# Performance work log

Hardware: AMD Instinct MI355X
Metric: run time of the kernel (lower is better)

The kernel has to match this reference:

```python
import jax, jax.numpy as jnp
import numpy as np

B, S, D, H = 4, 2048, 1024, 16
DH = D // H
NEG = -10000.0


def setup_inputs() -> dict:
    key = jax.random.key(0)
    ks = jax.random.split(key, 12)
    scale = 0.02
    inp = {
        "q": jax.random.normal(ks[0], (B, S, D), jnp.float32),
        "k": jax.random.normal(ks[1], (B, S, D), jnp.float32),
        "v": jax.random.normal(ks[2], (B, S, D), jnp.float32),
        "mask": jnp.triu(jnp.ones((S, S), jnp.bool_), k=1),  # True = masked (causal)
        "Wq": jax.random.normal(ks[3], (D, D), jnp.float32) * scale,
        "bq": jnp.zeros((D,), jnp.float32),
        "Wk": jax.random.normal(ks[4], (D, D), jnp.float32) * scale,
        "bk": jnp.zeros((D,), jnp.float32),
        "Wv": jax.random.normal(ks[5], (D, D), jnp.float32) * scale,
        "bv": jnp.zeros((D,), jnp.float32),
        "Wo": jax.random.normal(ks[6], (D, D), jnp.float32) * scale,
        "bo": jnp.zeros((D,), jnp.float32),
    }
    return inp


def _split(x):
    # [B,S,D] -> [B,H,S,DH]
    return x.reshape(B, S, H, DH).transpose(0, 2, 1, 3)


def reference(q, k, v, mask, Wq, bq, Wk, bk, Wv, bv, Wo, bo):
    # torch Linear: y = x @ W.T + b
    qh = _split(q @ Wq.T + bq)
    kh = _split(k @ Wk.T + bk)
    vh = _split(v @ Wv.T + bv)
    # scaled dot-product scores: [B,H,S,S]
    scores = jnp.einsum("bhqd,bhkd->bhqk", qh, kh) / jnp.sqrt(jnp.float32(DH))
    scores = scores + jnp.where(mask, jnp.float32(NEG), jnp.float32(0.0))
    attn = jax.nn.softmax(scores, axis=-1)  # dropout_rate=0 -> identity
    out = jnp.einsum("bhqk,bhkd->bhqd", attn, vh)
    out = out.transpose(0, 2, 1, 3).reshape(B, S, D)
    return out @ Wo.T + bo
```

## Files before the change

kernel.cpp:

```cpp
#include <hip/hip_runtime.h>
#include <hip/hip_bf16.h>


#define B_ 4
#define S_ 2048
#define D_ 1024
#define H_ 16
#define DH_ 64
#define M_ (B_*S_)
#define MASKADD (-14427.0f)
#define QSCALE  (0.180336880f)

typedef __attribute__((ext_vector_type(8)))  __bf16 bf16x8;
typedef __attribute__((ext_vector_type(8)))  unsigned short ushort8;
typedef __attribute__((ext_vector_type(4)))  float f32x4;
typedef __attribute__((ext_vector_type(16))) float f32x16;

__device__ __forceinline__ unsigned short f2bf(float f) {
  __hip_bfloat16 h = __float2bfloat16(f);
  union { __hip_bfloat16 h; unsigned short u; } c; c.h = h; return c.u;
}

__device__ __forceinline__ f32x4 mfma16(bf16x8 a, bf16x8 b, f32x4 c) {
  return __builtin_amdgcn_mfma_f32_16x16x32_bf16(a, b, c, 0, 0, 0);
}
__device__ __forceinline__ f32x16 mfma32(bf16x8 a, bf16x8 b, f32x16 c) {
  return __builtin_amdgcn_mfma_f32_32x32x16_bf16(a, b, c, 0, 0, 0);
}

__device__ __forceinline__ unsigned cvtpk(float lo, float hi) {
  unsigned r;
  asm("v_cvt_pk_bf16_f32 %0, %1, %2" : "=v"(r) : "v"(lo), "v"(hi));
  return r;
}

__device__ __forceinline__ void gld_lds16(const void* g, void* l) {
  __builtin_amdgcn_global_load_lds(
      (const __attribute__((address_space(1))) unsigned int*)g,
      (__attribute__((address_space(3))) unsigned int*)l, 16, 0, 0);
}

__global__ void cvt4_kernel(const float* __restrict__ p0, const float* __restrict__ p1,
                            const float* __restrict__ p2, const float* __restrict__ p3,
                            unsigned short* __restrict__ o0, unsigned short* __restrict__ o1,
                            unsigned short* __restrict__ o2, unsigned short* __restrict__ o3,
                            int n4) {
  int i = blockIdx.x * blockDim.x + threadIdx.x;
  if (i >= n4) return;
  const float* in  = (blockIdx.y == 0) ? p0 : (blockIdx.y == 1 ? p1 : (blockIdx.y == 2 ? p2 : p3));
  unsigned short* out = (blockIdx.y == 0) ? o0 : (blockIdx.y == 1 ? o1 : (blockIdx.y == 2 ? o2 : o3));
  float4 f = reinterpret_cast<const float4*>(in)[i];
  ushort4 o;
  o.x = f2bf(f.x); o.y = f2bf(f.y); o.z = f2bf(f.z); o.w = f2bf(f.w);
  reinterpret_cast<ushort4*>(out)[i] = o;
}

template<bool F32A>
__device__ __forceinline__
void gemm_body(const void* __restrict__ Ap, const unsigned short* __restrict__ W,
               const float* __restrict__ bias, void* __restrict__ outp,
               int mode, bool sc,
               unsigned short (*sA)[128*32], unsigned short (*sB)[128*32])
{
  const int tid  = threadIdx.x;
  const int lane = tid & 63, wid = tid >> 6;
  const int bx = blockIdx.x;
  const int j8 = bx & 7, i8 = bx >> 3;
  const int mt = j8*8 + (i8 >> 3), nt = i8 & 7;
  const int m0 = mt*128, n0 = nt*128;
  const int wr = wid >> 1, wc = wid & 1;

  const float* A32 = (const float*)Ap;
  const unsigned short* A16 = (const unsigned short*)Ap;

  f32x4 acc[4][4];
  #pragma unroll
  for (int i = 0; i < 4; ++i)
    #pragma unroll
    for (int j = 0; j < 4; ++j)
      #pragma unroll
      for (int r = 0; r < 4; ++r) acc[i][j][r] = 0.0f;

  auto stageB = [&](int bufi, int kt) {
    const unsigned short* Wb = W + (size_t)n0*D_ + kt*32;
    #pragma unroll
    for (int p = 0; p < 2; ++p) {
      int r = 32*wid + 16*p + (lane >> 2);
      int c = (lane & 3) * 8;
      gld_lds16(Wb + (size_t)r*D_ + c, &sB[bufi][(32*wid + 16*p)*32]);
    }
  };
  auto stageA16 = [&](int bufi, int kt) {
    const unsigned short* Ab = A16 + (size_t)m0*D_ + kt*32;
    #pragma unroll
    for (int p = 0; p < 2; ++p) {
      int r = 32*wid + 16*p + (lane >> 2);
      int c = (lane & 3) * 8;
      gld_lds16(Ab + (size_t)r*D_ + c, &sA[bufi][(32*wid + 16*p)*32]);
    }
  };

  f32x4 fr[4];
  auto loadA32 = [&](int kt) {
    const float* p = A32 + (size_t)(m0 + (tid >> 1))*D_ + kt*32 + (tid & 1)*16;
    fr[0] = *(const f32x4*)(p);
    fr[1] = *(const f32x4*)(p + 4);
    fr[2] = *(const f32x4*)(p + 8);
    fr[3] = *(const f32x4*)(p + 12);
  };
  auto writeA32 = [&](int bufi) {
    ushort8 o0, o1;
    #pragma unroll
    for (int j = 0; j < 4; ++j) {
      o0[j]   = f2bf(fr[0][j]);
      o0[4+j] = f2bf(fr[1][j]);
      o1[j]   = f2bf(fr[2][j]);
      o1[4+j] = f2bf(fr[3][j]);
    }
    unsigned short* dst = &sA[bufi][(tid >> 1)*32 + (tid & 1)*16];
    *(ushort8*)dst       = o0;
    *(ushort8*)(dst + 8) = o1;
  };

  if (F32A) { loadA32(0); writeA32(0); }
  else      { stageA16(0, 0); }
  stageB(0, 0);

  const int NK = D_/32;
  int buf = 0;
  for (int kt = 0; kt < NK; ++kt) {
    __syncthreads();
    bf16x8 aF[4], bF[4];
    #pragma unroll
    for (int i = 0; i < 4; ++i)
      aF[i] = *(const bf16x8*)&sA[buf][(64*wr + 16*i + (lane & 15))*32 + (lane >> 4)*8];
    #pragma unroll
    for (int j = 0; j < 4; ++j)
      bF[j] = *(const bf16x8*)&sB[buf][(64*wc + 16*j + (lane & 15))*32 + (lane >> 4)*8];

    if (kt + 1 < NK) {
      if (F32A) loadA32(kt + 1);
      else      stageA16(buf ^ 1, kt + 1);
      stageB(buf ^ 1, kt + 1);
    }

    #pragma unroll
    for (int i = 0; i < 4; ++i)
      #pragma unroll
      for (int j = 0; j < 4; ++j)
        acc[i][j] = mfma16(aF[i], bF[j], acc[i][j]);

    if (F32A && kt + 1 < NK) writeA32(buf ^ 1);
    buf ^= 1;
  }

  #pragma unroll
  for (int i = 0; i < 4; ++i) {
    int gr0 = m0 + 64*wr + 16*i + ((lane >> 4) << 2);
    #pragma unroll
    for (int j = 0; j < 4; ++j) {
      int gc = n0 + 64*wc + 16*j + (lane & 15);
      float bv = bias[gc];
      if (mode == 2) {
        int b = gr0 >> 11, s = gr0 & (S_ - 1);
        int hh = gc >> 6, dh = gc & (DH_ - 1);
        ushort4 o;
        o.x = f2bf(acc[i][j][0] + bv); o.y = f2bf(acc[i][j][1] + bv);
        o.z = f2bf(acc[i][j][2] + bv); o.w = f2bf(acc[i][j][3] + bv);
        *(ushort4*)&((unsigned short*)outp)[(((size_t)b*H_ + hh)*DH_ + dh)*S_ + s] = o;
      } else {
        #pragma unroll
        for (int r = 0; r < 4; ++r) {
          float v = acc[i][j][r] + bv;
          if (sc) v *= QSCALE;
          int gr = gr0 + r;
          if (mode == 0) {
            int b = gr >> 11, s = gr & (S_ - 1);
            int hh = gc >> 6, dh = gc & (DH_ - 1);
            ((unsigned short*)outp)[(((size_t)b*H_ + hh)*S_ + s)*DH_ + dh] = f2bf(v);
          } else {
            ((float*)outp)[(size_t)gr*D_ + gc] = v;
          }
        }
      }
    }
  }
}

__global__ __launch_bounds__(256, 2)
void gemm_qkv(const float* __restrict__ Aq, const float* __restrict__ Ak,
              const float* __restrict__ Av,
              const unsigned short* __restrict__ Wq_, const unsigned short* __restrict__ Wk_,
              const unsigned short* __restrict__ Wv_,
              const float* __restrict__ bq_, const float* __restrict__ bk_,
              const float* __restrict__ bv_,
              unsigned short* __restrict__ Oq, unsigned short* __restrict__ Ok,
              unsigned short* __restrict__ Ov)
{
  __shared__ unsigned short sA[2][128*32];
  __shared__ unsigned short sB[2][128*32];
  const int y = blockIdx.y;
  const float* A = (y == 0) ? Aq : (y == 1 ? Ak : Av);
  const unsigned short* W = (y == 0) ? Wq_ : (y == 1 ? Wk_ : Wv_);
  const float* bias        = (y == 0) ? bq_ : (y == 1 ? bk_ : bv_);
  unsigned short* outp     = (y == 0) ? Oq  : (y == 1 ? Ok  : Ov);
  gemm_body<true>(A, W, bias, outp, (y == 2) ? 2 : 0, y == 0, sA, sB);
}

__global__ __launch_bounds__(256, 2)
void gemm_out(const unsigned short* __restrict__ A, const unsigned short* __restrict__ W,
              const float* __restrict__ bias, float* __restrict__ outp)
{
  __shared__ unsigned short sA[2][128*32];
  __shared__ unsigned short sB[2][128*32];
  gemm_body<false>(A, W, bias, outp, 1, false, sA, sB);
}

__global__ __launch_bounds__(256)
void attn_kernel(const unsigned short* __restrict__ Qh, const unsigned short* __restrict__ Kh,
                 const unsigned short* __restrict__ Vt, unsigned short* __restrict__ AO)
{
  __shared__ unsigned short sK [2][64*64];
  __shared__ unsigned short sVt[2][64*64];

  const int tid = threadIdx.x, lane = tid & 63, wid = tid >> 6;
  const int l31 = lane & 31, h5 = lane >> 5;
  const int bh = blockIdx.x;
  const int chunk = 15 - (int)blockIdx.y;
  const int bb = bh >> 4, hd = bh & 15;
  const unsigned short* Qb = Qh + (size_t)bh * S_ * DH_;
  const unsigned short* Kb = Kh + (size_t)bh * S_ * DH_;
  const unsigned short* Vb = Vt + (size_t)bh * DH_ * S_;
  const int qc0 = chunk * 128;
  const int NT  = 2*chunk + 2;
  const int qw0 = qc0 + wid*32;
  const int q   = qw0 + l31;

  bf16x8 qF[4];
  #pragma unroll
  for (int c = 0; c < 4; ++c)
    qF[c] = *(const bf16x8*)(Qb + (size_t)q*DH_ + c*16 + h5*8);

  f32x16 zz;
  #pragma unroll
  for (int r = 0; r < 16; ++r) zz[r] = 0.0f;
  f32x16 accO0 = zz, accO1 = zz;
  float lsum = 0.0f;

  auto stageK = [&](int bufi, int t) {
    #pragma unroll
    for (int p = 0; p < 2; ++p) {
      int ch = 2*wid + p;
      int row = ch*8 + (lane >> 3);
      int cbs = ((lane & 7) * 16) ^ ((row & 7) << 4);
      gld_lds16(Kb + (size_t)(t*64 + row)*DH_ + (cbs >> 1), &sK[bufi][ch*512]);
    }
  };
  auto stageV = [&](int bufi, int t) {
    #pragma unroll
    for (int p = 0; p < 2; ++p) {
      int ch = 2*wid + p;
      int row = ch*8 + (lane >> 3);
      int cbs = ((lane & 7) * 16) ^ ((row & 7) << 4);
      gld_lds16(Vb + (size_t)row*S_ + t*64 + (cbs >> 1), &sVt[bufi][ch*512]);
    }
  };

  stageK(0, 0);
  stageV(0, 0);

  int buf = 0;
  for (int t = 0; t < NT; ++t) {
    __syncthreads();
    if (t + 1 < NT) { stageK(buf ^ 1, t + 1); stageV(buf ^ 1, t + 1); }

    #pragma unroll
    for (int sub = 0; sub < 2; ++sub) {
      const int kv0 = t*64 + sub*32;
      if (kv0 > qw0 + 31) continue;
      const bool dodiag = (kv0 + 31 > qw0);

      f32x16 st = zz;
      __builtin_amdgcn_s_setprio(1);
      #pragma unroll
      for (int c = 0; c < 4; ++c) {
        int row = sub*32 + l31;
        const char* base = (const char*)&sK[buf][0] + row*128;
        bf16x8 kf = *(const bf16x8*)(base + ((32*c + 16*h5) ^ ((row & 7) << 4)));
        st = mfma32(kf, qF[c], st);
      }
      __builtin_amdgcn_s_setprio(0);

      #pragma unroll
      for (int r = 0; r < 16; ++r) {
        float x = st[r];
        if (dodiag) {
          int kv = kv0 + (r & 3) + 8*(r >> 2) + 4*h5;
          if (kv > q) x += MASKADD;
        }
        x = __builtin_amdgcn_exp2f(x);
        st[r] = x;
        lsum += x;
      }

      #pragma unroll
      for (int hh = 0; hh < 2; ++hh) {
        union { unsigned u[4]; bf16x8 v; } pb;
        pb.u[0] = cvtpk(st[8*hh+0], st[8*hh+1]);
        pb.u[1] = cvtpk(st[8*hh+2], st[8*hh+3]);
        pb.u[2] = cvtpk(st[8*hh+4], st[8*hh+5]);
        pb.u[3] = cvtpk(st[8*hh+6], st[8*hh+7]);

        __builtin_amdgcn_s_setprio(1);
        #pragma unroll
        for (int dh = 0; dh < 2; ++dh) {
          int row = dh*32 + l31;
          const char* base = (const char*)&sVt[buf][0] + row*128;
          int sw = (row & 7) << 4;
          int X = 64*sub + 32*hh + 8*h5;
          union { uint2 g[2]; bf16x8 v; } vv;
          vv.g[0] = *(const uint2*)(base + ((X)      ^ sw));
          vv.g[1] = *(const uint2*)(base + ((X + 16) ^ sw));
          if (dh == 0) accO0 = mfma32(vv.v, pb.v, accO0);
          else         accO1 = mfma32(vv.v, pb.v, accO1);
        }
        __builtin_amdgcn_s_setprio(0);
      }
    }
    buf ^= 1;
  }

  float lt = lsum + __shfl_xor(lsum, 32, 64);
  float inv = 1.0f / lt;
  unsigned short* ao = AO + ((size_t)bb*S_ + q)*D_ + hd*DH_;
  #pragma unroll
  for (int dh = 0; dh < 2; ++dh) {
    const f32x16 A = dh ? accO1 : accO0;
    #pragma unroll
    for (int rq = 0; rq < 4; ++rq) {
      ushort4 o;
      o.x = f2bf(A[4*rq+0] * inv);
      o.y = f2bf(A[4*rq+1] * inv);
      o.z = f2bf(A[4*rq+2] * inv);
      o.w = f2bf(A[4*rq+3] * inv);
      int dbase = dh*32 + 8*rq + 4*h5;
      *(ushort4*)&ao[dbase] = o;
    }
  }
}

extern "C" void kernel_launch(void* const* d_in, const int* in_sizes, int n_in,
                              void* d_out, int out_size, void* d_ws, size_t ws_size,
                              hipStream_t stream)
{
  const float* q  = (const float*)d_in[0];
  const float* k  = (const float*)d_in[1];
  const float* v  = (const float*)d_in[2];
  const float* Wq = (const float*)d_in[4];
  const float* bq = (const float*)d_in[5];
  const float* Wk = (const float*)d_in[6];
  const float* bk = (const float*)d_in[7];
  const float* Wv = (const float*)d_in[8];
  const float* bv = (const float*)d_in[9];
  const float* Wo = (const float*)d_in[10];
  const float* bo = (const float*)d_in[11];

  unsigned short* ws = (unsigned short*)d_ws;
  const size_t MD = (size_t)M_ * D_;
  const size_t DD = (size_t)D_ * D_;
  unsigned short* Wqb = ws;
  unsigned short* Wkb = Wqb + DD;
  unsigned short* Wvb = Wkb + DD;
  unsigned short* Wob = Wvb + DD;
  unsigned short* Qhb = Wob + DD;
  unsigned short* Khb = Qhb + MD;
  unsigned short* Vtb = Khb + MD;
  unsigned short* AOb = Vtb + MD;

  cvt4_kernel<<<dim3((int)(DD/4/256), 4), 256, 0, stream>>>(Wq, Wk, Wv, Wo, Wqb, Wkb, Wvb, Wob, (int)(DD/4));

  gemm_qkv<<<dim3(512, 3), 256, 0, stream>>>(q, k, v, Wqb, Wkb, Wvb,
                                             bq, bk, bv, Qhb, Khb, Vtb);

  attn_kernel<<<dim3(64, 16), 256, 0, stream>>>(Qhb, Khb, Vtb, AOb);

  gemm_out<<<512, 256, 0, stream>>>(AOb, Wob, bo, (float*)d_out);
}
```

Measured before the change: 190.7 us.

## Stage fp32 A tiles directly into LDS asynchronously and convert at fragment load

The QKV projection GEMM previously loaded fp32 activations into registers, converted them to bf16 and wrote them to LDS after the MFMAs. It now uses direct global-to-LDS loads of raw fp32 data into an XOR-swizzled LDS buffer, issued before the fragment reads, and converts to bf16 with packed converts when building the MFMA A fragments. This is meant to remove register staging and the write-after-compute step and to overlap A loads like the B loads. In exchange LDS use for A doubles and each wave repeats the conversion work, which may affect occupancy and ALU load.

```diff
diff --git a/kernel.cpp b/kernel.cpp
--- a/kernel.cpp
+++ b/kernel.cpp
@@ -60,7 +60,7 @@
 void gemm_body(const void* __restrict__ Ap, const unsigned short* __restrict__ W,
                const float* __restrict__ bias, void* __restrict__ outp,
                int mode, bool sc,
-               unsigned short (*sA)[128*32], unsigned short (*sB)[128*32])
+               unsigned short* sA16, float* sA32, unsigned short* sB)
 {
   const int tid  = threadIdx.x;
   const int lane = tid & 63, wid = tid >> 6;
@@ -69,6 +69,7 @@
   const int mt = j8*8 + (i8 >> 3), nt = i8 & 7;
   const int m0 = mt*128, n0 = nt*128;
   const int wr = wid >> 1, wc = wid & 1;
+  const int g = lane >> 4;
 
   const float* A32 = (const float*)Ap;
   const unsigned short* A16 = (const unsigned short*)Ap;
@@ -87,7 +88,7 @@
     for (int p = 0; p < 2; ++p) {
       int r = 32*wid + 16*p + (lane >> 2);
       int c = (lane & 3) * 8;
-      gld_lds16(Wb + (size_t)r*D_ + c, &sB[bufi][(32*wid + 16*p)*32]);
+      gld_lds16(Wb + (size_t)r*D_ + c, &sB[bufi*4096 + (32*wid + 16*p)*32]);
     }
   };
   auto stageA16 = [&](int bufi, int kt) {
@@ -96,61 +97,61 @@
     for (int p = 0; p < 2; ++p) {
       int r = 32*wid + 16*p + (lane >> 2);
       int c = (lane & 3) * 8;
-      gld_lds16(Ab + (size_t)r*D_ + c, &sA[bufi][(32*wid + 16*p)*32]);
-    }
-  };
-
-  f32x4 fr[4];
-  auto loadA32 = [&](int kt) {
-    const float* p = A32 + (size_t)(m0 + (tid >> 1))*D_ + kt*32 + (tid & 1)*16;
-    fr[0] = *(const f32x4*)(p);
-    fr[1] = *(const f32x4*)(p + 4);
-    fr[2] = *(const f32x4*)(p + 8);
-    fr[3] = *(const f32x4*)(p + 12);
-  };
-  auto writeA32 = [&](int bufi) {
-    ushort8 o0, o1;
-    #pragma unroll
-    for (int j = 0; j < 4; ++j) {
-      o0[j]   = f2bf(fr[0][j]);
-      o0[4+j] = f2bf(fr[1][j]);
-      o1[j]   = f2bf(fr[2][j]);
-      o1[4+j] = f2bf(fr[3][j]);
-    }
-    unsigned short* dst = &sA[bufi][(tid >> 1)*32 + (tid & 1)*16];
-    *(ushort8*)dst       = o0;
-    *(ushort8*)(dst + 8) = o1;
-  };
-
-  if (F32A) { loadA32(0); writeA32(0); }
-  else      { stageA16(0, 0); }
+      gld_lds16(Ab + (size_t)r*D_ + c, &sA16[bufi*4096 + (32*wid + 16*p)*32]);
+    }
+  };
+  auto stageA32 = [&](int bufi, int kt) {
+    const float* Ab = A32 + (size_t)m0*D_ + kt*32;
+    #pragma unroll
+    for (int p = 0; p < 4; ++p) {
+      int ch = 4*wid + p;
+      int row = ch*8 + (lane >> 3);
+      int cbs = ((lane & 7) * 16) ^ ((lane >> 3) << 4);
+      gld_lds16(Ab + (size_t)row*D_ + (cbs >> 2), &sA32[bufi*4096 + ch*256]);
+    }
+  };
+
+  if (F32A) stageA32(0, 0); else stageA16(0, 0);
   stageB(0, 0);
 
   const int NK = D_/32;
   int buf = 0;
   for (int kt = 0; kt < NK; ++kt) {
     __syncthreads();
-    bf16x8 aF[4], bF[4];
-    #pragma unroll
-    for (int i = 0; i < 4; ++i)
-      aF[i] = *(const bf16x8*)&sA[buf][(64*wr + 16*i + (lane & 15))*32 + (lane >> 4)*8];
-    #pragma unroll
-    for (int j = 0; j < 4; ++j)
-      bF[j] = *(const bf16x8*)&sB[buf][(64*wc + 16*j + (lane & 15))*32 + (lane >> 4)*8];
-
     if (kt + 1 < NK) {
-      if (F32A) loadA32(kt + 1);
+      if (F32A) stageA32(buf ^ 1, kt + 1);
       else      stageA16(buf ^ 1, kt + 1);
       stageB(buf ^ 1, kt + 1);
     }
 
+    bf16x8 aF[4], bF[4];
+    #pragma unroll
+    for (int i = 0; i < 4; ++i) {
+      int row = 64*wr + 16*i + (lane & 15);
+      if (F32A) {
+        const char* base = (const char*)(sA32 + buf*4096) + row*128;
+        int sw = (row & 7) << 4;
+        f32x4 a0 = *(const f32x4*)(base + ((g*32)      ^ sw));
+        f32x4 a1 = *(const f32x4*)(base + ((g*32 + 16) ^ sw));
+        union { unsigned u[4]; bf16x8 v; } af;
+        af.u[0] = cvtpk(a0[0], a0[1]);
+        af.u[1] = cvtpk(a0[2], a0[3]);
+        af.u[2] = cvtpk(a1[0], a1[1]);
+        af.u[3] = cvtpk(a1[2], a1[3]);
+        aF[i] = af.v;
+      } else {
+        aF[i] = *(const bf16x8*)&sA16[buf*4096 + row*32 + g*8];
+      }
+    }
+    #pragma unroll
+    for (int j = 0; j < 4; ++j)
+      bF[j] = *(const bf16x8*)&sB[buf*4096 + (64*wc + 16*j + (lane & 15))*32 + g*8];
+
     #pragma unroll
     for (int i = 0; i < 4; ++i)
       #pragma unroll
       for (int j = 0; j < 4; ++j)
         acc[i][j] = mfma16(aF[i], bF[j], acc[i][j]);
-
-    if (F32A && kt + 1 < NK) writeA32(buf ^ 1);
     buf ^= 1;
   }
 
@@ -197,23 +198,23 @@
               unsigned short* __restrict__ Oq, unsigned short* __restrict__ Ok,
               unsigned short* __restrict__ Ov)
 {
-  __shared__ unsigned short sA[2][128*32];
-  __shared__ unsigned short sB[2][128*32];
+  __shared__ float          sA32[2*4096];
+  __shared__ unsigned short sB  [2*4096];
   const int y = blockIdx.y;
   const float* A = (y == 0) ? Aq : (y == 1 ? Ak : Av);
   const unsigned short* W = (y == 0) ? Wq_ : (y == 1 ? Wk_ : Wv_);
   const float* bias        = (y == 0) ? bq_ : (y == 1 ? bk_ : bv_);
   unsigned short* outp     = (y == 0) ? Oq  : (y == 1 ? Ok  : Ov);
-  gemm_body<true>(A, W, bias, outp, (y == 2) ? 2 : 0, y == 0, sA, sB);
+  gemm_body<true>(A, W, bias, outp, (y == 2) ? 2 : 0, y == 0, nullptr, sA32, sB);
 }
 
 __global__ __launch_bounds__(256, 2)
 void gemm_out(const unsigned short* __restrict__ A, const unsigned short* __restrict__ W,
               const float* __restrict__ bias, float* __restrict__ outp)
 {
-  __shared__ unsigned short sA[2][128*32];
-  __shared__ unsigned short sB[2][128*32];
-  gemm_body<false>(A, W, bias, outp, 1, false, sA, sB);
+  __shared__ unsigned short sA16[2*4096];
+  __shared__ unsigned short sB  [2*4096];
+  gemm_body<false>(A, W, bias, outp, 1, false, sA16, nullptr, sB);
 }
 
 __global__ __launch_bounds__(256)
```

Measured after the change: 175.4 us. -8.0%, faster.
